# Performance work log

Measured on AMD Instinct MI355X. Metric: run time of the kernel, lower is better.

Reference implementation:

```python
import jax, jax.numpy as jnp
import numpy as np

N_LEAVES = 16384
D = 1024
L = 32


def _build_full_binary_tree(n_leaves):
    # Leaves are node ids [0, n_leaves); internal nodes are assigned ids level by
    # level bottom-up, so children always have smaller ids than their parent and
    # left_idx/right_idx are grouped contiguously per level.
    level_nodes = np.arange(n_leaves)
    nid = n_leaves
    lefts, rights = [], []
    while level_nodes.size > 1:
        lefts.append(level_nodes[0::2])
        rights.append(level_nodes[1::2])
        w = level_nodes.size // 2
        level_nodes = np.arange(nid, nid + w)
        nid += w
    return np.concatenate(lefts).astype(np.int32), np.concatenate(rights).astype(np.int32)


def setup_inputs() -> dict:
    key = jax.random.key(0)
    k_h, k_t, k_w = jax.random.split(key, 3)
    n_nodes = 2 * N_LEAVES - 1
    hidden = jax.random.normal(k_h, (n_nodes, D), dtype=jnp.float32)
    # xavier_normal-ish scales
    trans = jax.random.normal(k_t, (L, L), dtype=jnp.float32) * (2.0 / (L + L)) ** 0.5
    W_pred = jax.random.normal(k_w, (L, 2 * D), dtype=jnp.float32) * (2.0 / (2 * D + L)) ** 0.5
    b_pred = jnp.zeros((L,), dtype=jnp.float32)
    left_idx, right_idx = _build_full_binary_tree(N_LEAVES)
    return {
        "hidden": hidden,
        "trans": trans,
        "W_pred": W_pred,
        "b_pred": b_pred,
        "left_idx": jnp.asarray(left_idx),
        "right_idx": jnp.asarray(right_idx),
    }


def reference(hidden, trans, W_pred, b_pred, left_idx, right_idx):
    # hidden: [N, D] node bottom-up hidden states; N = 2*n_leaves - 1
    n_nodes, d = hidden.shape
    n_leaves = (n_nodes + 1) // 2
    num_labels = trans.shape[0]

    # collect_avg_hidden: mean over all node hidden states
    avg_h = jnp.mean(hidden, axis=0)  # [D]
    # avg_h_pred: emission = Linear(concat(h, avg_h))  -> [N, L]
    feats = jnp.concatenate(
        [hidden, jnp.broadcast_to(avg_h, hidden.shape)], axis=1
    )  # [N, 2D]
    emission = feats @ W_pred.T + b_pred  # [N, L]

    # Inside DP, bottom-up, batched by tree level. For an internal node p:
    #   inside[p, y] = logsumexp_{l,r}( emission[p,y] + trans[y,l] + inside_left[l]
    #                                   + trans[y,r] + inside_right[r] )
    # which factorizes exactly into two independent logsumexps.
    scores = jnp.zeros((n_nodes, num_labels), dtype=hidden.dtype)
    scores = scores.at[:n_leaves].set(emission[:n_leaves])

    pos = 0
    node_base = n_leaves
    width = n_leaves // 2
    while width >= 1:  # fixed log2(n_leaves) structural levels
        li = left_idx[pos:pos + width]
        ri = right_idx[pos:pos + width]
        ls = scores[li]  # [width, L]
        rs = scores[ri]  # [width, L]
        # trans[y, c] + child_score[c], logsumexp over child label c
        left_m = jax.nn.logsumexp(trans[None, :, :] + ls[:, None, :], axis=2)
        right_m = jax.nn.logsumexp(trans[None, :, :] + rs[:, None, :], axis=2)
        new = emission[node_base:node_base + width] + left_m + right_m
        scores = scores.at[node_base:node_base + width].set(new)
        pos += width
        node_base += width
        width //= 2

    return scores[n_nodes - 1]  # root inside score, [L]
```

## Files before the change

### kernel.cpp

```cpp
#include <hip/hip_runtime.h>

#define NN 32767
#define NL 16384
#define DD 1024
#define LL 32

typedef __attribute__((ext_vector_type(8))) short bf16x8;
typedef __attribute__((ext_vector_type(4))) float f32x4;

__device__ __forceinline__ short f2bf(float f) {
  union { float f; unsigned u; } x; x.f = f;
  unsigned r = x.u + 0x7FFFu + ((x.u >> 16) & 1u);
  return (short)(r >> 16);
}

__device__ __forceinline__ bf16x8 cvt8(float4 a, float4 b) {
  bf16x8 r;
  r[0] = f2bf(a.x); r[1] = f2bf(a.y); r[2] = f2bf(a.z); r[3] = f2bf(a.w);
  r[4] = f2bf(b.x); r[5] = f2bf(b.y); r[6] = f2bf(b.z); r[7] = f2bf(b.w);
  return r;
}

__device__ __forceinline__ void gld_lds16(const float* g, float* l) {
  __builtin_amdgcn_global_load_lds(
      (const __attribute__((address_space(1))) void*)g,
      (__attribute__((address_space(3))) void*)l, 16, 0, 0);
}

__global__ __launch_bounds__(256) void pack_kernel(const float* __restrict__ Wp,
                                                   short* __restrict__ Wpk) {
  int idx = blockIdx.x * 256 + threadIdx.x;
  #pragma unroll
  for (int t = 0; t < 4; ++t, idx += 16384) {
    const int j = idx & 7, m = (idx >> 3) & 3, lane = (idx >> 5) & 63, s = idx >> 11;
    const int wrow = (lane & 15) + 16 * (m & 1);
    const int wcol = (m >> 1) * 1024 + s * 32 + (lane >> 4) * 8 + j;
    Wpk[idx] = f2bf(Wp[(size_t)wrow * (2 * DD) + wcol]);
  }
}

__global__ __launch_bounds__(256) void gemm_kernel(
    const float* __restrict__ hidden, const short* __restrict__ Wpk,
    float* __restrict__ E0, float* __restrict__ gpart) {
  __shared__ float lds[4 * 3 * 1024];
  const int tid = threadIdx.x;
  const int wid = tid >> 6, lane = tid & 63;
  const int tile = blockIdx.x * 4 + wid;
  const int mrow = lane & 15, g = lane >> 4;
  const int swz = (mrow & 7) << 4;
  float* ldsw = lds + wid * 3072;

  const float* ab0; const float* ab1; const float* ab2; const float* ab3;
  {
    const int lr = lane >> 4, lc16 = (lane & 15) * 16;
    #define MKAB(I, P) { const int row = (I)*4 + lr;                         \
      const int csrc = lc16 ^ ((row & 7) << 4);                              \
      int grow = tile * 16 + row; if (grow > NN - 1) grow = NN - 1;          \
      P = hidden + (size_t)grow * DD + (csrc >> 2); }
    MKAB(0, ab0) MKAB(1, ab1) MKAB(2, ab2) MKAB(3, ab3)
    #undef MKAB
  }
  const bf16x8* wbase = (const bf16x8*)Wpk + (size_t)lane * 4;

  const int cidx00 = ((g * 32) ^ swz) >> 2;
  const int cidx01 = ((g * 32 + 16) ^ swz) >> 2;
  const int cidx10 = ((128 + g * 32) ^ swz) >> 2;
  const int cidx11 = ((128 + g * 32 + 16) ^ swz) >> 2;

  f32x4 acc0 = {0,0,0,0}, acc1 = {0,0,0,0}, acc2 = {0,0,0,0}, acc3 = {0,0,0,0};

#define STAGE_A(KC) {                                   \
    float* ld_ = ldsw + ((KC) % 3) * 1024;              \
    gld_lds16(ab0 + (KC) * 64, ld_);                    \
    gld_lds16(ab1 + (KC) * 64, ld_ + 256);              \
    gld_lds16(ab2 + (KC) * 64, ld_ + 512);              \
    gld_lds16(ab3 + (KC) * 64, ld_ + 768); }

#define LOAD_W(KC, W0,W1,W2,W3, X0,X1,X2,X3) {          \
    const bf16x8* p_ = wbase + (size_t)(2 * (KC)) * 256; \
    W0 = p_[0];   W1 = p_[1];   W2 = p_[2];   W3 = p_[3]; \
    X0 = p_[256]; X1 = p_[257]; X2 = p_[258]; X3 = p_[259]; }

#define CHUNK(KC, VM, W0,W1,W2,W3, X0,X1,X2,X3)                              \
  { if ((KC) + 2 < 16) STAGE_A((KC) + 2)                                     \
    asm volatile("s_waitcnt vmcnt(" VM ")" ::: "memory");                    \
    { const float* bc = ldsw + ((KC) % 3) * 1024 + mrow * 64;                \
      float4 fa0 = *(const float4*)(bc + cidx00);                            \
      float4 fb0 = *(const float4*)(bc + cidx01);                            \
      bf16x8 af0 = cvt8(fa0, fb0);                                           \
      acc0 = __builtin_amdgcn_mfma_f32_16x16x32_bf16(af0, W0, acc0, 0,0,0);  \
      acc1 = __builtin_amdgcn_mfma_f32_16x16x32_bf16(af0, W1, acc1, 0,0,0);  \
      acc2 = __builtin_amdgcn_mfma_f32_16x16x32_bf16(af0, W2, acc2, 0,0,0);  \
      acc3 = __builtin_amdgcn_mfma_f32_16x16x32_bf16(af0, W3, acc3, 0,0,0);  \
      float4 fa1 = *(const float4*)(bc + cidx10);                            \
      float4 fb1 = *(const float4*)(bc + cidx11);                            \
      bf16x8 af1 = cvt8(fa1, fb1);                                           \
      acc0 = __builtin_amdgcn_mfma_f32_16x16x32_bf16(af1, X0, acc0, 0,0,0);  \
      acc1 = __builtin_amdgcn_mfma_f32_16x16x32_bf16(af1, X1, acc1, 0,0,0);  \
      acc2 = __builtin_amdgcn_mfma_f32_16x16x32_bf16(af1, X2, acc2, 0,0,0);  \
      acc3 = __builtin_amdgcn_mfma_f32_16x16x32_bf16(af1, X3, acc3, 0,0,0);  \
    }                                                                        \
    if ((KC) + 2 < 16) LOAD_W((KC) + 2, W0,W1,W2,W3, X0,X1,X2,X3) }

  bf16x8 u0,u1,u2,u3,u4,u5,u6,u7, v0,v1,v2,v3,v4,v5,v6,v7;
  STAGE_A(0) STAGE_A(1)
  LOAD_W(0, u0,u1,u2,u3, u4,u5,u6,u7)
  LOAD_W(1, v0,v1,v2,v3, v4,v5,v6,v7)
  CHUNK( 0, "24", u0,u1,u2,u3, u4,u5,u6,u7)
  CHUNK( 1, "32", v0,v1,v2,v3, v4,v5,v6,v7)
  CHUNK( 2, "24", u0,u1,u2,u3, u4,u5,u6,u7)
  CHUNK( 3, "24", v0,v1,v2,v3, v4,v5,v6,v7)
  CHUNK( 4, "24", u0,u1,u2,u3, u4,u5,u6,u7)
  CHUNK( 5, "24", v0,v1,v2,v3, v4,v5,v6,v7)
  CHUNK( 6, "24", u0,u1,u2,u3, u4,u5,u6,u7)
  CHUNK( 7, "24", v0,v1,v2,v3, v4,v5,v6,v7)
  CHUNK( 8, "24", u0,u1,u2,u3, u4,u5,u6,u7)
  CHUNK( 9, "24", v0,v1,v2,v3, v4,v5,v6,v7)
  CHUNK(10, "24", u0,u1,u2,u3, u4,u5,u6,u7)
  CHUNK(11, "24", v0,v1,v2,v3, v4,v5,v6,v7)
  CHUNK(12, "24", u0,u1,u2,u3, u4,u5,u6,u7)
  CHUNK(13, "24", v0,v1,v2,v3, v4,v5,v6,v7)
  CHUNK(14, "20", u0,u1,u2,u3, u4,u5,u6,u7)
  CHUNK(15, "8",  v0,v1,v2,v3, v4,v5,v6,v7)
#undef CHUNK
#undef LOAD_W
#undef STAGE_A

  #pragma unroll
  for (int r = 0; r < 4; ++r) {
    const int srow = tile * 16 + g * 4 + r;
    if (srow < NN) {
      E0[(size_t)srow * LL + mrow]      = acc0[r];
      E0[(size_t)srow * LL + mrow + 16] = acc1[r];
    }
  }
  if (tile == 2047 && g == 3) { acc2[3] = 0.f; acc3[3] = 0.f; }
  float s2 = acc2[0] + acc2[1] + acc2[2] + acc2[3];
  float s3 = acc3[0] + acc3[1] + acc3[2] + acc3[3];
  s2 += __shfl_xor(s2, 16, 64); s2 += __shfl_xor(s2, 32, 64);
  s3 += __shfl_xor(s3, 16, 64); s3 += __shfl_xor(s3, 32, 64);
  if (lane < 32) gpart[(size_t)tile * LL + lane] = (lane < 16) ? s2 : s3;
}

__global__ __launch_bounds__(256) void cvec_kernel(
    const float* __restrict__ bp, const float* __restrict__ gpart,
    float* __restrict__ cvec) {
  const int col = blockIdx.x;
  const int tid = threadIdx.x, wid = tid >> 6, lane = tid & 63;
  float s = 0.f;
  for (int w = tid; w < 2048; w += 256) s += gpart[(size_t)w * LL + col];
  #pragma unroll
  for (int m = 1; m <= 32; m <<= 1) s += __shfl_xor(s, m, 64);
  __shared__ float red[4];
  if (lane == 0) red[wid] = s;
  __syncthreads();
  if (tid == 0)
    cvec[col] = bp[col] + (red[0] + red[1] + red[2] + red[3]) * (1.0f / (float)NN);
}

__device__ __forceinline__ float lse32(const float4* tt, const float4* sv) {
  float m = -3.0e38f;
  float4 v[8];
  #pragma unroll
  for (int i = 0; i < 8; ++i) {
    float4 t = tt[i], s = sv[i], w;
    w.x = t.x + s.x; w.y = t.y + s.y; w.z = t.z + s.z; w.w = t.w + s.w;
    v[i] = w;
    m = fmaxf(m, fmaxf(fmaxf(w.x, w.y), fmaxf(w.z, w.w)));
  }
  float ss = 0.f;
  #pragma unroll
  for (int i = 0; i < 8; ++i) {
    ss += __expf(v[i].x - m) + __expf(v[i].y - m) +
          __expf(v[i].z - m) + __expf(v[i].w - m);
  }
  return m + __logf(ss);
}

__global__ __launch_bounds__(1024) void tree_kernel(
    const float* __restrict__ E0, const float* __restrict__ cvec,
    const float* __restrict__ trans, const float* __restrict__ src,
    float* __restrict__ dst, int base1, int leafmode) {
  __shared__ float l1[16][LL], l2[8][LL], l3[4][LL];
  const int wid = threadIdx.x >> 6, lane = threadIdx.x & 63;
  const int j = lane & 31, half = lane >> 5;
  const int b = blockIdx.x, G = gridDim.x;
  float4 tt[8];
  #pragma unroll
  for (int i = 0; i < 8; ++i) tt[i] = *(const float4*)(trans + j * LL + i * 4);
  const float cj = cvec[j];
  float4 sv[8];

  {
    const int n = b * 16 + wid;
    const float* sp = src + (size_t)(2 * n + half) * LL;
    if (leafmode) {
      #pragma unroll
      for (int i = 0; i < 8; ++i) {
        float4 vv = *(const float4*)(sp + i * 4);
        float4 c4 = *(const float4*)(cvec + i * 4);
        vv.x += c4.x; vv.y += c4.y; vv.z += c4.z; vv.w += c4.w;
        sv[i] = vv;
      }
    } else {
      #pragma unroll
      for (int i = 0; i < 8; ++i) sv[i] = *(const float4*)(sp + i * 4);
    }
    float lsum = lse32(tt, sv);
    float other = __shfl_xor(lsum, 32, 64);
    float o = E0[(size_t)(base1 + n) * LL + j] + cj + lsum + other;
    if (lane < 32) l1[wid][j] = o;
  }
  __syncthreads();
  const int base2 = base1 + G * 16;
  if (wid < 8) {
    const float* sp = l1[2 * wid + half];
    #pragma unroll
    for (int i = 0; i < 8; ++i) sv[i] = *(const float4*)(sp + i * 4);
    float lsum = lse32(tt, sv);
    float other = __shfl_xor(lsum, 32, 64);
    float o = E0[(size_t)(base2 + b * 8 + wid) * LL + j] + cj + lsum + other;
    if (lane < 32) l2[wid][j] = o;
  }
  __syncthreads();
  const int base3 = base2 + G * 8;
  if (wid < 4) {
    const float* sp = l2[2 * wid + half];
    #pragma unroll
    for (int i = 0; i < 8; ++i) sv[i] = *(const float4*)(sp + i * 4);
    float lsum = lse32(tt, sv);
    float other = __shfl_xor(lsum, 32, 64);
    float o = E0[(size_t)(base3 + b * 4 + wid) * LL + j] + cj + lsum + other;
    if (lane < 32) l3[wid][j] = o;
  }
  __syncthreads();
  const int base4 = base3 + G * 4;
  if (wid < 2) {
    const float* sp = l3[2 * wid + half];
    #pragma unroll
    for (int i = 0; i < 8; ++i) sv[i] = *(const float4*)(sp + i * 4);
    float lsum = lse32(tt, sv);
    float other = __shfl_xor(lsum, 32, 64);
    float o = E0[(size_t)(base4 + b * 2 + wid) * LL + j] + cj + lsum + other;
    if (lane < 32) l1[wid][j] = o;
  }
  __syncthreads();
  const int base5 = base4 + G * 2;
  if (wid == 0) {
    const float* sp = l1[half];
    #pragma unroll
    for (int i = 0; i < 8; ++i) sv[i] = *(const float4*)(sp + i * 4);
    float lsum = lse32(tt, sv);
    float other = __shfl_xor(lsum, 32, 64);
    float o = E0[(size_t)(base5 + b) * LL + j] + cj + lsum + other;
    if (lane < 32) dst[(size_t)b * LL + j] = o;
  }
}

__global__ __launch_bounds__(512) void tail_kernel(
    const float* __restrict__ E0, const float* __restrict__ cvec,
    const float* __restrict__ trans, const float* __restrict__ S10,
    float* __restrict__ out) {
  __shared__ float t1[8][LL], t2[4][LL], t3[2][LL];
  const int wid = threadIdx.x >> 6, lane = threadIdx.x & 63;
  const int j = lane & 31, half = lane >> 5;
  float4 tt[8];
  #pragma unroll
  for (int i = 0; i < 8; ++i) tt[i] = *(const float4*)(trans + j * LL + i * 4);
  const float cj = cvec[j];
  float4 sv[8];

  {
    const float* sp = S10 + (size_t)(2 * wid + half) * LL;
    #pragma unroll
    for (int i = 0; i < 8; ++i) sv[i] = *(const float4*)(sp + i * 4);
    float lsum = lse32(tt, sv);
    float other = __shfl_xor(lsum, 32, 64);
    float o = E0[(size_t)(32752 + wid) * LL + j] + cj + lsum + other;
    if (lane < 32) t1[wid][j] = o;
  }
  __syncthreads();
  if (wid < 4) {
    const float* sp = t1[2 * wid + half];
    #pragma unroll
    for (int i = 0; i < 8; ++i) sv[i] = *(const float4*)(sp + i * 4);
    float lsum = lse32(tt, sv);
    float other = __shfl_xor(lsum, 32, 64);
    float o = E0[(size_t)(32760 + wid) * LL + j] + cj + lsum + other;
    if (lane < 32) t2[wid][j] = o;
  }
  __syncthreads();
  if (wid < 2) {
    const float* sp = t2[2 * wid + half];
    #pragma unroll
    for (int i = 0; i < 8; ++i) sv[i] = *(const float4*)(sp + i * 4);
    float lsum = lse32(tt, sv);
    float other = __shfl_xor(lsum, 32, 64);
    float o = E0[(size_t)(32764 + wid) * LL + j] + cj + lsum + other;
    if (lane < 32) t3[wid][j] = o;
  }
  __syncthreads();
  if (wid == 0) {
    const float* sp = t3[half];
    #pragma unroll
    for (int i = 0; i < 8; ++i) sv[i] = *(const float4*)(sp + i * 4);
    float lsum = lse32(tt, sv);
    float other = __shfl_xor(lsum, 32, 64);
    float o = E0[(size_t)32766 * LL + j] + cj + lsum + other;
    if (lane < 32) out[j] = o;
  }
}

extern "C" void kernel_launch(void* const* d_in, const int* in_sizes, int n_in,
                              void* d_out, int out_size, void* d_ws, size_t ws_size,
                              hipStream_t stream) {
  const float* hidden = (const float*)d_in[0];
  const float* trans  = (const float*)d_in[1];
  const float* Wp     = (const float*)d_in[2];
  const float* bp     = (const float*)d_in[3];

  float* ws    = (float*)d_ws;
  float* E0    = ws;
  float* gpart = E0 + (size_t)NN * LL;
  float* cvecb = gpart + (size_t)2048 * LL;
  float* S5    = cvecb + 32;
  float* S10   = S5 + 512 * LL;
  short* Wpk   = (short*)(S10 + 16 * LL);

  pack_kernel<<<64, 256, 0, stream>>>(Wp, Wpk);
  gemm_kernel<<<512, 256, 0, stream>>>(hidden, Wpk, E0, gpart);
  cvec_kernel<<<32, 256, 0, stream>>>(bp, gpart, cvecb);
  tree_kernel<<<512, 1024, 0, stream>>>(E0, cvecb, trans, E0, S5, 16384, 1);
  tree_kernel<<<16, 1024, 0, stream>>>(E0, cvecb, trans, S5, S10, 32256, 0);
  tail_kernel<<<1, 512, 0, stream>>>(E0, cvecb, trans, S10, (float*)d_out);
}
```

Before: 73.26 us.

## Split GEMM K across waves, drop LDS staging, fuse cvec reduction into tree kernels

The GEMM kernel now uses 1024-thread blocks in which two groups of waves each handle half of K. Each wave loads hidden directly from global memory into registers instead of staging through LDS with async copies, and the two halves are combined through shared memory. Per-block column sums are reduced to 256 partials, and the separate cvec kernel is removed: each tree and tail block recomputes cvec from those partials. This saves one launch and the LDS pipeline, but adds redundant reduction work in every tree block and loses the explicit prefetch overlap.

```diff
diff --git a/kernel.cpp b/kernel.cpp
--- a/kernel.cpp
+++ b/kernel.cpp
@@ -21,12 +21,6 @@
   return r;
 }
 
-__device__ __forceinline__ void gld_lds16(const float* g, float* l) {
-  __builtin_amdgcn_global_load_lds(
-      (const __attribute__((address_space(1))) void*)g,
-      (__attribute__((address_space(3))) void*)l, 16, 0, 0);
-}
-
 __global__ __launch_bounds__(256) void pack_kernel(const float* __restrict__ Wp,
                                                    short* __restrict__ Wpk) {
   int idx = blockIdx.x * 256 + threadIdx.x;
@@ -39,123 +33,80 @@
   }
 }
 
-__global__ __launch_bounds__(256) void gemm_kernel(
+__global__ __launch_bounds__(1024, 4) void gemm_kernel(
     const float* __restrict__ hidden, const short* __restrict__ Wpk,
-    float* __restrict__ E0, float* __restrict__ gpart) {
-  __shared__ float lds[4 * 3 * 1024];
+    float* __restrict__ E0, float* __restrict__ gpartB) {
+  __shared__ float cmb[8 * 1024];
+  __shared__ float part2[8][LL];
   const int tid = threadIdx.x;
   const int wid = tid >> 6, lane = tid & 63;
-  const int tile = blockIdx.x * 4 + wid;
+  const int wt = wid & 7, kh = wid >> 3;
+  const int tile = blockIdx.x * 8 + wt;
   const int mrow = lane & 15, g = lane >> 4;
-  const int swz = (mrow & 7) << 4;
-  float* ldsw = lds + wid * 3072;
-
-  const float* ab0; const float* ab1; const float* ab2; const float* ab3;
-  {
-    const int lr = lane >> 4, lc16 = (lane & 15) * 16;
-    #define MKAB(I, P) { const int row = (I)*4 + lr;                         \
-      const int csrc = lc16 ^ ((row & 7) << 4);                              \
-      int grow = tile * 16 + row; if (grow > NN - 1) grow = NN - 1;          \
-      P = hidden + (size_t)grow * DD + (csrc >> 2); }
-    MKAB(0, ab0) MKAB(1, ab1) MKAB(2, ab2) MKAB(3, ab3)
-    #undef MKAB
-  }
-  const bf16x8* wbase = (const bf16x8*)Wpk + (size_t)lane * 4;
-
-  const int cidx00 = ((g * 32) ^ swz) >> 2;
-  const int cidx01 = ((g * 32 + 16) ^ swz) >> 2;
-  const int cidx10 = ((128 + g * 32) ^ swz) >> 2;
-  const int cidx11 = ((128 + g * 32 + 16) ^ swz) >> 2;
+  int grow = tile * 16 + mrow;
+  if (grow > NN - 1) grow = NN - 1;
+
+  const float*  ap = hidden + (size_t)grow * DD + kh * 512 + g * 8;
+  const bf16x8* wb = (const bf16x8*)Wpk + kh * 4096 + lane * 4;
 
   f32x4 acc0 = {0,0,0,0}, acc1 = {0,0,0,0}, acc2 = {0,0,0,0}, acc3 = {0,0,0,0};
 
-#define STAGE_A(KC) {                                   \
-    float* ld_ = ldsw + ((KC) % 3) * 1024;              \
-    gld_lds16(ab0 + (KC) * 64, ld_);                    \
-    gld_lds16(ab1 + (KC) * 64, ld_ + 256);              \
-    gld_lds16(ab2 + (KC) * 64, ld_ + 512);              \
-    gld_lds16(ab3 + (KC) * 64, ld_ + 768); }
-
-#define LOAD_W(KC, W0,W1,W2,W3, X0,X1,X2,X3) {          \
-    const bf16x8* p_ = wbase + (size_t)(2 * (KC)) * 256; \
-    W0 = p_[0];   W1 = p_[1];   W2 = p_[2];   W3 = p_[3]; \
-    X0 = p_[256]; X1 = p_[257]; X2 = p_[258]; X3 = p_[259]; }
-
-#define CHUNK(KC, VM, W0,W1,W2,W3, X0,X1,X2,X3)                              \
-  { if ((KC) + 2 < 16) STAGE_A((KC) + 2)                                     \
-    asm volatile("s_waitcnt vmcnt(" VM ")" ::: "memory");                    \
-    { const float* bc = ldsw + ((KC) % 3) * 1024 + mrow * 64;                \
-      float4 fa0 = *(const float4*)(bc + cidx00);                            \
-      float4 fb0 = *(const float4*)(bc + cidx01);                            \
-      bf16x8 af0 = cvt8(fa0, fb0);                                           \
-      acc0 = __builtin_amdgcn_mfma_f32_16x16x32_bf16(af0, W0, acc0, 0,0,0);  \
-      acc1 = __builtin_amdgcn_mfma_f32_16x16x32_bf16(af0, W1, acc1, 0,0,0);  \
-      acc2 = __builtin_amdgcn_mfma_f32_16x16x32_bf16(af0, W2, acc2, 0,0,0);  \
-      acc3 = __builtin_amdgcn_mfma_f32_16x16x32_bf16(af0, W3, acc3, 0,0,0);  \
-      float4 fa1 = *(const float4*)(bc + cidx10);                            \
-      float4 fb1 = *(const float4*)(bc + cidx11);                            \
-      bf16x8 af1 = cvt8(fa1, fb1);                                           \
-      acc0 = __builtin_amdgcn_mfma_f32_16x16x32_bf16(af1, X0, acc0, 0,0,0);  \
-      acc1 = __builtin_amdgcn_mfma_f32_16x16x32_bf16(af1, X1, acc1, 0,0,0);  \
-      acc2 = __builtin_amdgcn_mfma_f32_16x16x32_bf16(af1, X2, acc2, 0,0,0);  \
-      acc3 = __builtin_amdgcn_mfma_f32_16x16x32_bf16(af1, X3, acc3, 0,0,0);  \
-    }                                                                        \
-    if ((KC) + 2 < 16) LOAD_W((KC) + 2, W0,W1,W2,W3, X0,X1,X2,X3) }
-
-  bf16x8 u0,u1,u2,u3,u4,u5,u6,u7, v0,v1,v2,v3,v4,v5,v6,v7;
-  STAGE_A(0) STAGE_A(1)
-  LOAD_W(0, u0,u1,u2,u3, u4,u5,u6,u7)
-  LOAD_W(1, v0,v1,v2,v3, v4,v5,v6,v7)
-  CHUNK( 0, "24", u0,u1,u2,u3, u4,u5,u6,u7)
-  CHUNK( 1, "32", v0,v1,v2,v3, v4,v5,v6,v7)
-  CHUNK( 2, "24", u0,u1,u2,u3, u4,u5,u6,u7)
-  CHUNK( 3, "24", v0,v1,v2,v3, v4,v5,v6,v7)
-  CHUNK( 4, "24", u0,u1,u2,u3, u4,u5,u6,u7)
-  CHUNK( 5, "24", v0,v1,v2,v3, v4,v5,v6,v7)
-  CHUNK( 6, "24", u0,u1,u2,u3, u4,u5,u6,u7)
-  CHUNK( 7, "24", v0,v1,v2,v3, v4,v5,v6,v7)
-  CHUNK( 8, "24", u0,u1,u2,u3, u4,u5,u6,u7)
-  CHUNK( 9, "24", v0,v1,v2,v3, v4,v5,v6,v7)
-  CHUNK(10, "24", u0,u1,u2,u3, u4,u5,u6,u7)
-  CHUNK(11, "24", v0,v1,v2,v3, v4,v5,v6,v7)
-  CHUNK(12, "24", u0,u1,u2,u3, u4,u5,u6,u7)
-  CHUNK(13, "24", v0,v1,v2,v3, v4,v5,v6,v7)
-  CHUNK(14, "20", u0,u1,u2,u3, u4,u5,u6,u7)
-  CHUNK(15, "8",  v0,v1,v2,v3, v4,v5,v6,v7)
-#undef CHUNK
-#undef LOAD_W
-#undef STAGE_A
-
-  #pragma unroll
-  for (int r = 0; r < 4; ++r) {
-    const int srow = tile * 16 + g * 4 + r;
-    if (srow < NN) {
-      E0[(size_t)srow * LL + mrow]      = acc0[r];
-      E0[(size_t)srow * LL + mrow + 16] = acc1[r];
+  #pragma unroll
+  for (int c = 0; c < 8; ++c) {
+    float4 a0 = *(const float4*)(ap + c * 64);
+    float4 a1 = *(const float4*)(ap + c * 64 + 4);
+    float4 a2 = *(const float4*)(ap + c * 64 + 32);
+    float4 a3 = *(const float4*)(ap + c * 64 + 36);
+    const bf16x8* p = wb + c * 512;
+    bf16x8 w0 = p[0],   w1 = p[1],   w2 = p[2],   w3 = p[3];
+    bf16x8 x0 = p[256], x1 = p[257], x2 = p[258], x3 = p[259];
+    bf16x8 af0 = cvt8(a0, a1);
+    acc0 = __builtin_amdgcn_mfma_f32_16x16x32_bf16(af0, w0, acc0, 0, 0, 0);
+    acc1 = __builtin_amdgcn_mfma_f32_16x16x32_bf16(af0, w1, acc1, 0, 0, 0);
+    acc2 = __builtin_amdgcn_mfma_f32_16x16x32_bf16(af0, w2, acc2, 0, 0, 0);
+    acc3 = __builtin_amdgcn_mfma_f32_16x16x32_bf16(af0, w3, acc3, 0, 0, 0);
+    bf16x8 af1 = cvt8(a2, a3);
+    acc0 = __builtin_amdgcn_mfma_f32_16x16x32_bf16(af1, x0, acc0, 0, 0, 0);
+    acc1 = __builtin_amdgcn_mfma_f32_16x16x32_bf16(af1, x1, acc1, 0, 0, 0);
+    acc2 = __builtin_amdgcn_mfma_f32_16x16x32_bf16(af1, x2, acc2, 0, 0, 0);
+    acc3 = __builtin_amdgcn_mfma_f32_16x16x32_bf16(af1, x3, acc3, 0, 0, 0);
+  }
+
+  float* cl = cmb + wt * 1024 + lane * 16;
+  if (kh == 1) {
+    *(f32x4*)(cl)      = acc0;
+    *(f32x4*)(cl + 4)  = acc1;
+    *(f32x4*)(cl + 8)  = acc2;
+    *(f32x4*)(cl + 12) = acc3;
+  }
+  __syncthreads();
+  if (kh == 0) {
+    acc0 += *(const f32x4*)(cl);
+    acc1 += *(const f32x4*)(cl + 4);
+    acc2 += *(const f32x4*)(cl + 8);
+    acc3 += *(const f32x4*)(cl + 12);
+    #pragma unroll
+    for (int r = 0; r < 4; ++r) {
+      const int srow = tile * 16 + g * 4 + r;
+      if (srow < NN) {
+        E0[(size_t)srow * LL + mrow]      = acc0[r];
+        E0[(size_t)srow * LL + mrow + 16] = acc1[r];
+      }
     }
-  }
-  if (tile == 2047 && g == 3) { acc2[3] = 0.f; acc3[3] = 0.f; }
-  float s2 = acc2[0] + acc2[1] + acc2[2] + acc2[3];
-  float s3 = acc3[0] + acc3[1] + acc3[2] + acc3[3];
-  s2 += __shfl_xor(s2, 16, 64); s2 += __shfl_xor(s2, 32, 64);
-  s3 += __shfl_xor(s3, 16, 64); s3 += __shfl_xor(s3, 32, 64);
-  if (lane < 32) gpart[(size_t)tile * LL + lane] = (lane < 16) ? s2 : s3;
-}
-
-__global__ __launch_bounds__(256) void cvec_kernel(
-    const float* __restrict__ bp, const float* __restrict__ gpart,
-    float* __restrict__ cvec) {
-  const int col = blockIdx.x;
-  const int tid = threadIdx.x, wid = tid >> 6, lane = tid & 63;
-  float s = 0.f;
-  for (int w = tid; w < 2048; w += 256) s += gpart[(size_t)w * LL + col];
-  #pragma unroll
-  for (int m = 1; m <= 32; m <<= 1) s += __shfl_xor(s, m, 64);
-  __shared__ float red[4];
-  if (lane == 0) red[wid] = s;
-  __syncthreads();
-  if (tid == 0)
-    cvec[col] = bp[col] + (red[0] + red[1] + red[2] + red[3]) * (1.0f / (float)NN);
+    if (tile == 2047 && g == 3) { acc2[3] = 0.f; acc3[3] = 0.f; }
+    float s2 = acc2[0] + acc2[1] + acc2[2] + acc2[3];
+    float s3 = acc3[0] + acc3[1] + acc3[2] + acc3[3];
+    s2 += __shfl_xor(s2, 16, 64); s2 += __shfl_xor(s2, 32, 64);
+    s3 += __shfl_xor(s3, 16, 64); s3 += __shfl_xor(s3, 32, 64);
+    if (lane < 32) part2[wt][lane] = (lane < 16) ? s2 : s3;
+  }
+  __syncthreads();
+  if (tid < LL) {
+    float s = 0.f;
+    #pragma unroll
+    for (int q = 0; q < 8; ++q) s += part2[q][tid];
+    gpartB[blockIdx.x * LL + tid] = s;
+  }
 }
 
 __device__ __forceinline__ float lse32(const float4* tt, const float4* sv) {
@@ -177,18 +128,42 @@
   return m + __logf(ss);
 }
 
+__device__ __forceinline__ void compute_cvec(const float* __restrict__ gpartB,
+                                             const float* __restrict__ bp,
+                                             float* cv, float (*pr)[LL]) {
+  const int tid = threadIdx.x;
+  const int j = tid & 31, r = tid >> 5;
+  float s = 0.f;
+  #pragma unroll
+  for (int q = 0; q < 8; ++q) s += gpartB[(size_t)(r + q * 32) * LL + j];
+  pr[r][j] = s;
+  __syncthreads();
+  if (tid < LL) {
+    float ss = 0.f;
+    #pragma unroll
+    for (int q = 0; q < 32; ++q) ss += pr[q][tid];
+    cv[tid] = bp[tid] + ss * (1.0f / (float)NN);
+  }
+  __syncthreads();
+}
+
 __global__ __launch_bounds__(1024) void tree_kernel(
-    const float* __restrict__ E0, const float* __restrict__ cvec,
-    const float* __restrict__ trans, const float* __restrict__ src,
-    float* __restrict__ dst, int base1, int leafmode) {
+    const float* __restrict__ E0, const float* __restrict__ gpartB,
+    const float* __restrict__ bp, const float* __restrict__ trans,
+    const float* __restrict__ src, float* __restrict__ dst,
+    int base1, int leafmode) {
+  __shared__ __align__(16) float cv[LL];
+  __shared__ float pr[32][LL];
   __shared__ float l1[16][LL], l2[8][LL], l3[4][LL];
+  compute_cvec(gpartB, bp, cv, pr);
+
   const int wid = threadIdx.x >> 6, lane = threadIdx.x & 63;
   const int j = lane & 31, half = lane >> 5;
   const int b = blockIdx.x, G = gridDim.x;
   float4 tt[8];
   #pragma unroll
   for (int i = 0; i < 8; ++i) tt[i] = *(const float4*)(trans + j * LL + i * 4);
-  const float cj = cvec[j];
+  const float cj = cv[j];
   float4 sv[8];
 
   {
@@ -198,7 +173,7 @@
       #pragma unroll
       for (int i = 0; i < 8; ++i) {
         float4 vv = *(const float4*)(sp + i * 4);
-        float4 c4 = *(const float4*)(cvec + i * 4);
+        float4 c4 = *(const float4*)(cv + i * 4);
         vv.x += c4.x; vv.y += c4.y; vv.z += c4.z; vv.w += c4.w;
         sv[i] = vv;
       }
@@ -257,20 +232,24 @@
   }
 }
 
-__global__ __launch_bounds__(512) void tail_kernel(
-    const float* __restrict__ E0, const float* __restrict__ cvec,
-    const float* __restrict__ trans, const float* __restrict__ S10,
-    float* __restrict__ out) {
+__global__ __launch_bounds__(1024) void tail_kernel(
+    const float* __restrict__ E0, const float* __restrict__ gpartB,
+    const float* __restrict__ bp, const float* __restrict__ trans,
+    const float* __restrict__ S10, float* __restrict__ out) {
+  __shared__ __align__(16) float cv[LL];
+  __shared__ float pr[32][LL];
   __shared__ float t1[8][LL], t2[4][LL], t3[2][LL];
+  compute_cvec(gpartB, bp, cv, pr);
+
   const int wid = threadIdx.x >> 6, lane = threadIdx.x & 63;
   const int j = lane & 31, half = lane >> 5;
   float4 tt[8];
   #pragma unroll
   for (int i = 0; i < 8; ++i) tt[i] = *(const float4*)(trans + j * LL + i * 4);
-  const float cj = cvec[j];
+  const float cj = cv[j];
   float4 sv[8];
 
-  {
+  if (wid < 8) {
     const float* sp = S10 + (size_t)(2 * wid + half) * LL;
     #pragma unroll
     for (int i = 0; i < 8; ++i) sv[i] = *(const float4*)(sp + i * 4);
@@ -319,18 +298,16 @@
   const float* Wp     = (const float*)d_in[2];
   const float* bp     = (const float*)d_in[3];
 
-  float* ws    = (float*)d_ws;
-  float* E0    = ws;
-  float* gpart = E0 + (size_t)NN * LL;
-  float* cvecb = gpart + (size_t)2048 * LL;
-  float* S5    = cvecb + 32;
-  float* S10   = S5 + 512 * LL;
-  short* Wpk   = (short*)(S10 + 16 * LL);
+  float* ws     = (float*)d_ws;
+  float* E0     = ws;
+  float* gpartB = E0 + (size_t)NN * LL;
+  float* S5     = gpartB + 256 * LL;
+  float* S10    = S5 + 512 * LL;
+  short* Wpk    = (short*)(S10 + 16 * LL);
 
   pack_kernel<<<64, 256, 0, stream>>>(Wp, Wpk);
-  gemm_kernel<<<512, 256, 0, stream>>>(hidden, Wpk, E0, gpart);
-  cvec_kernel<<<32, 256, 0, stream>>>(bp, gpart, cvecb);
-  tree_kernel<<<512, 1024, 0, stream>>>(E0, cvecb, trans, E0, S5, 16384, 1);
-  tree_kernel<<<16, 1024, 0, stream>>>(E0, cvecb, trans, S5, S10, 32256, 0);
-  tail_kernel<<<1, 512, 0, stream>>>(E0, cvecb, trans, S10, (float*)d_out);
-}
+  gemm_kernel<<<256, 1024, 0, stream>>>(hidden, Wpk, E0, gpartB);
+  tree_kernel<<<512, 1024, 0, stream>>>(E0, gpartB, bp, trans, E0, S5, 16384, 1);
+  tree_kernel<<<16, 1024, 0, stream>>>(E0, gpartB, bp, trans, S5, S10, 32256, 0);
+  tail_kernel<<<1, 1024, 0, stream>>>(E0, gpartB, bp, trans, S10, (float*)d_out);
+}
```

Result: slower. 81.77 us (+11.6%).

## Fuse cvec reduction and tree tail into last-block-done epilogues

Applied to the files above, without the earlier changes.

Removes the separate cvec, second tree and tail kernel launches. The GEMM's last-finishing block, detected with an atomic counter, now reduces the per-block column sums into cvec. The tree kernel's last block finishes the top nine tree levels in LDS. This cuts three launches and their inter-kernel gaps, at the cost of serialising the top levels on one block, adding atomic/fence overhead, and a large LDS allocation for every tree block.

```diff
diff --git a/kernel.cpp b/kernel.cpp
--- a/kernel.cpp
+++ b/kernel.cpp
@@ -1,4 +1,5 @@
 #include <hip/hip_runtime.h>
+
 
 #define NN 32767
 #define NL 16384
@@ -28,7 +29,9 @@
 }
 
 __global__ __launch_bounds__(256) void pack_kernel(const float* __restrict__ Wp,
-                                                   short* __restrict__ Wpk) {
+                                                   short* __restrict__ Wpk,
+                                                   unsigned* __restrict__ cnt) {
+  if (blockIdx.x == 0 && threadIdx.x == 0) { cnt[0] = 0u; cnt[1] = 0u; }
   int idx = blockIdx.x * 256 + threadIdx.x;
   #pragma unroll
   for (int t = 0; t < 4; ++t, idx += 16384) {
@@ -41,8 +44,13 @@
 
 __global__ __launch_bounds__(256) void gemm_kernel(
     const float* __restrict__ hidden, const short* __restrict__ Wpk,
-    float* __restrict__ E0, float* __restrict__ gpart) {
+    const float* __restrict__ bp, float* __restrict__ E0,
+    float* __restrict__ gpartB, float* __restrict__ cvec,
+    unsigned* __restrict__ cnt) {
   __shared__ float lds[4 * 3 * 1024];
+  __shared__ float part2[4][LL];
+  __shared__ float partC[8][LL];
+  __shared__ bool amLast;
   const int tid = threadIdx.x;
   const int wid = tid >> 6, lane = tid & 63;
   const int tile = blockIdx.x * 4 + wid;
@@ -139,23 +147,32 @@
   float s3 = acc3[0] + acc3[1] + acc3[2] + acc3[3];
   s2 += __shfl_xor(s2, 16, 64); s2 += __shfl_xor(s2, 32, 64);
   s3 += __shfl_xor(s3, 16, 64); s3 += __shfl_xor(s3, 32, 64);
-  if (lane < 32) gpart[(size_t)tile * LL + lane] = (lane < 16) ? s2 : s3;
-}
-
-__global__ __launch_bounds__(256) void cvec_kernel(
-    const float* __restrict__ bp, const float* __restrict__ gpart,
-    float* __restrict__ cvec) {
-  const int col = blockIdx.x;
-  const int tid = threadIdx.x, wid = tid >> 6, lane = tid & 63;
-  float s = 0.f;
-  for (int w = tid; w < 2048; w += 256) s += gpart[(size_t)w * LL + col];
-  #pragma unroll
-  for (int m = 1; m <= 32; m <<= 1) s += __shfl_xor(s, m, 64);
-  __shared__ float red[4];
-  if (lane == 0) red[wid] = s;
-  __syncthreads();
-  if (tid == 0)
-    cvec[col] = bp[col] + (red[0] + red[1] + red[2] + red[3]) * (1.0f / (float)NN);
+  if (lane < 32) part2[wid][lane] = (lane < 16) ? s2 : s3;
+  __syncthreads();
+  if (tid < LL) {
+    gpartB[blockIdx.x * LL + tid] =
+        part2[0][tid] + part2[1][tid] + part2[2][tid] + part2[3][tid];
+  }
+  __syncthreads();
+  if (tid == 0) {
+    __threadfence();
+    unsigned old = atomicAdd(&cnt[0], 1u);
+    amLast = (old == 511u);
+  }
+  __syncthreads();
+  if (amLast) {
+    __threadfence();
+    const int col = tid & 31, rg = tid >> 5;
+    float s = 0.f;
+    for (int r = rg; r < 512; r += 8) s += gpartB[(size_t)r * LL + col];
+    partC[rg][col] = s;
+    __syncthreads();
+    if (tid < LL) {
+      float ss = partC[0][tid] + partC[1][tid] + partC[2][tid] + partC[3][tid] +
+                 partC[4][tid] + partC[5][tid] + partC[6][tid] + partC[7][tid];
+      cvec[tid] = bp[tid] + ss * (1.0f / (float)NN);
+    }
+  }
 }
 
 __device__ __forceinline__ float lse32(const float4* tt, const float4* sv) {
@@ -179,9 +196,11 @@
 
 __global__ __launch_bounds__(1024) void tree_kernel(
     const float* __restrict__ E0, const float* __restrict__ cvec,
-    const float* __restrict__ trans, const float* __restrict__ src,
-    float* __restrict__ dst, int base1, int leafmode) {
+    const float* __restrict__ trans, float* __restrict__ S5,
+    float* __restrict__ out, unsigned* __restrict__ cnt) {
   __shared__ float l1[16][LL], l2[8][LL], l3[4][LL];
+  __shared__ float ts[511 * LL];
+  __shared__ bool amLast;
   const int wid = threadIdx.x >> 6, lane = threadIdx.x & 63;
   const int j = lane & 31, half = lane >> 5;
   const int b = blockIdx.x, G = gridDim.x;
@@ -190,21 +209,17 @@
   for (int i = 0; i < 8; ++i) tt[i] = *(const float4*)(trans + j * LL + i * 4);
   const float cj = cvec[j];
   float4 sv[8];
+  const int base1 = NL;
 
   {
     const int n = b * 16 + wid;
-    const float* sp = src + (size_t)(2 * n + half) * LL;
-    if (leafmode) {
-      #pragma unroll
-      for (int i = 0; i < 8; ++i) {
-        float4 vv = *(const float4*)(sp + i * 4);
-        float4 c4 = *(const float4*)(cvec + i * 4);
-        vv.x += c4.x; vv.y += c4.y; vv.z += c4.z; vv.w += c4.w;
-        sv[i] = vv;
-      }
-    } else {
-      #pragma unroll
-      for (int i = 0; i < 8; ++i) sv[i] = *(const float4*)(sp + i * 4);
+    const float* sp = E0 + (size_t)(2 * n + half) * LL;
+    #pragma unroll
+    for (int i = 0; i < 8; ++i) {
+      float4 vv = *(const float4*)(sp + i * 4);
+      float4 c4 = *(const float4*)(cvec + i * 4);
+      vv.x += c4.x; vv.y += c4.y; vv.z += c4.z; vv.w += c4.w;
+      sv[i] = vv;
     }
     float lsum = lse32(tt, sv);
     float other = __shfl_xor(lsum, 32, 64);
@@ -253,61 +268,39 @@
     float lsum = lse32(tt, sv);
     float other = __shfl_xor(lsum, 32, 64);
     float o = E0[(size_t)(base5 + b) * LL + j] + cj + lsum + other;
-    if (lane < 32) dst[(size_t)b * LL + j] = o;
-  }
-}
-
-__global__ __launch_bounds__(512) void tail_kernel(
-    const float* __restrict__ E0, const float* __restrict__ cvec,
-    const float* __restrict__ trans, const float* __restrict__ S10,
-    float* __restrict__ out) {
-  __shared__ float t1[8][LL], t2[4][LL], t3[2][LL];
-  const int wid = threadIdx.x >> 6, lane = threadIdx.x & 63;
-  const int j = lane & 31, half = lane >> 5;
-  float4 tt[8];
-  #pragma unroll
-  for (int i = 0; i < 8; ++i) tt[i] = *(const float4*)(trans + j * LL + i * 4);
-  const float cj = cvec[j];
-  float4 sv[8];
-
-  {
-    const float* sp = S10 + (size_t)(2 * wid + half) * LL;
-    #pragma unroll
-    for (int i = 0; i < 8; ++i) sv[i] = *(const float4*)(sp + i * 4);
-    float lsum = lse32(tt, sv);
-    float other = __shfl_xor(lsum, 32, 64);
-    float o = E0[(size_t)(32752 + wid) * LL + j] + cj + lsum + other;
-    if (lane < 32) t1[wid][j] = o;
-  }
-  __syncthreads();
-  if (wid < 4) {
-    const float* sp = t1[2 * wid + half];
-    #pragma unroll
-    for (int i = 0; i < 8; ++i) sv[i] = *(const float4*)(sp + i * 4);
-    float lsum = lse32(tt, sv);
-    float other = __shfl_xor(lsum, 32, 64);
-    float o = E0[(size_t)(32760 + wid) * LL + j] + cj + lsum + other;
-    if (lane < 32) t2[wid][j] = o;
-  }
-  __syncthreads();
-  if (wid < 2) {
-    const float* sp = t2[2 * wid + half];
-    #pragma unroll
-    for (int i = 0; i < 8; ++i) sv[i] = *(const float4*)(sp + i * 4);
-    float lsum = lse32(tt, sv);
-    float other = __shfl_xor(lsum, 32, 64);
-    float o = E0[(size_t)(32764 + wid) * LL + j] + cj + lsum + other;
-    if (lane < 32) t3[wid][j] = o;
-  }
-  __syncthreads();
-  if (wid == 0) {
-    const float* sp = t3[half];
-    #pragma unroll
-    for (int i = 0; i < 8; ++i) sv[i] = *(const float4*)(sp + i * 4);
-    float lsum = lse32(tt, sv);
-    float other = __shfl_xor(lsum, 32, 64);
-    float o = E0[(size_t)32766 * LL + j] + cj + lsum + other;
-    if (lane < 32) out[j] = o;
+    if (lane < 32) S5[(size_t)b * LL + j] = o;
+  }
+  __syncthreads();
+  if (threadIdx.x == 0) {
+    __threadfence();
+    unsigned old = atomicAdd(&cnt[1], 1u);
+    amLast = (old == 511u);
+  }
+  __syncthreads();
+  if (!amLast) return;
+  __threadfence();
+
+  int width = 256, pnode = 32256, cIdxBase = -1;
+  while (width >= 1) {
+    for (int n = wid; n < width; n += 16) {
+      const float* sp = (cIdxBase < 0)
+          ? (S5 + (size_t)(2 * n + half) * LL)
+          : (ts + (size_t)(cIdxBase + 2 * n + half) * LL);
+      #pragma unroll
+      for (int i = 0; i < 8; ++i) sv[i] = *(const float4*)(sp + i * 4);
+      float lsum = lse32(tt, sv);
+      float other = __shfl_xor(lsum, 32, 64);
+      if (lane < 32) {
+        const int node = pnode + n;
+        float o = E0[(size_t)node * LL + j] + cj + lsum + other;
+        ts[(size_t)(node - 32256) * LL + j] = o;
+        if (node == NN - 1) out[j] = o;
+      }
+    }
+    __syncthreads();
+    cIdxBase = pnode - 32256;
+    pnode += width;
+    width >>= 1;
   }
 }
 
@@ -319,18 +312,15 @@
   const float* Wp     = (const float*)d_in[2];
   const float* bp     = (const float*)d_in[3];
 
-  float* ws    = (float*)d_ws;
-  float* E0    = ws;
-  float* gpart = E0 + (size_t)NN * LL;
-  float* cvecb = gpart + (size_t)2048 * LL;
-  float* S5    = cvecb + 32;
-  float* S10   = S5 + 512 * LL;
-  short* Wpk   = (short*)(S10 + 16 * LL);
-
-  pack_kernel<<<64, 256, 0, stream>>>(Wp, Wpk);
-  gemm_kernel<<<512, 256, 0, stream>>>(hidden, Wpk, E0, gpart);
-  cvec_kernel<<<32, 256, 0, stream>>>(bp, gpart, cvecb);
-  tree_kernel<<<512, 1024, 0, stream>>>(E0, cvecb, trans, E0, S5, 16384, 1);
-  tree_kernel<<<16, 1024, 0, stream>>>(E0, cvecb, trans, S5, S10, 32256, 0);
-  tail_kernel<<<1, 512, 0, stream>>>(E0, cvecb, trans, S10, (float*)d_out);
-}
+  float* ws     = (float*)d_ws;
+  float* E0     = ws;
+  float* gpartB = E0 + (size_t)NN * LL;
+  float* cvecb  = gpartB + 512 * LL;
+  float* S5     = cvecb + 32;
+  short* Wpk    = (short*)(S5 + 512 * LL);
+  unsigned* cnt = (unsigned*)(Wpk + 65536);
+
+  pack_kernel<<<64, 256, 0, stream>>>(Wp, Wpk, cnt);
+  gemm_kernel<<<512, 256, 0, stream>>>(hidden, Wpk, bp, E0, gpartB, cvecb, cnt);
+  tree_kernel<<<512, 1024, 0, stream>>>(E0, cvecb, trans, S5, (float*)d_out, cnt);
+}
```

New measurement: 153.7 us. 110% more time.

## Fuse cvec reduction into tree kernels and collapse tree levels into two launches

Applied to the files above, without the earlier changes.

Removes the separate cvec reduction kernel. Each tree block now recomputes the column-mean vector from gpart in shared memory. The tree DP is regrouped into one 256-block kernel covering six levels and one single-block tail kernel covering the remaining eight levels, down from three tree launches. This cuts launch count and inter-kernel gaps, at the cost of redundant cvec work in every block and fewer blocks in the first tree stage.

```diff
diff --git a/kernel.cpp b/kernel.cpp
--- a/kernel.cpp
+++ b/kernel.cpp
@@ -1,4 +1,5 @@
 #include <hip/hip_runtime.h>
+
 
 #define NN 32767
 #define NL 16384
@@ -142,22 +143,6 @@
   if (lane < 32) gpart[(size_t)tile * LL + lane] = (lane < 16) ? s2 : s3;
 }
 
-__global__ __launch_bounds__(256) void cvec_kernel(
-    const float* __restrict__ bp, const float* __restrict__ gpart,
-    float* __restrict__ cvec) {
-  const int col = blockIdx.x;
-  const int tid = threadIdx.x, wid = tid >> 6, lane = tid & 63;
-  float s = 0.f;
-  for (int w = tid; w < 2048; w += 256) s += gpart[(size_t)w * LL + col];
-  #pragma unroll
-  for (int m = 1; m <= 32; m <<= 1) s += __shfl_xor(s, m, 64);
-  __shared__ float red[4];
-  if (lane == 0) red[wid] = s;
-  __syncthreads();
-  if (tid == 0)
-    cvec[col] = bp[col] + (red[0] + red[1] + red[2] + red[3]) * (1.0f / (float)NN);
-}
-
 __device__ __forceinline__ float lse32(const float4* tt, const float4* sv) {
   float m = -3.0e38f;
   float4 v[8];
@@ -177,137 +162,149 @@
   return m + __logf(ss);
 }
 
-__global__ __launch_bounds__(1024) void tree_kernel(
-    const float* __restrict__ E0, const float* __restrict__ cvec,
-    const float* __restrict__ trans, const float* __restrict__ src,
-    float* __restrict__ dst, int base1, int leafmode) {
-  __shared__ float l1[16][LL], l2[8][LL], l3[4][LL];
+__device__ __forceinline__ void compute_cvec(const float* __restrict__ gpart,
+                                             const float* __restrict__ bp,
+                                             float* cv, float (*pr)[LL]) {
+  const int tid = threadIdx.x;
+  const int j = tid & 31, r = tid >> 5;
+  float s = 0.f;
+  #pragma unroll 8
+  for (int q = 0; q < 64; ++q) s += gpart[(size_t)(r + q * 32) * LL + j];
+  pr[r][j] = s;
+  __syncthreads();
+  if (tid < LL) {
+    float ss = 0.f;
+    #pragma unroll
+    for (int q = 0; q < 32; ++q) ss += pr[q][tid];
+    cv[tid] = bp[tid] + ss * (1.0f / (float)NN);
+  }
+  __syncthreads();
+}
+
+__global__ __launch_bounds__(1024) void treeA_kernel(
+    const float* __restrict__ E0, const float* __restrict__ gpart,
+    const float* __restrict__ bp, const float* __restrict__ trans,
+    float* __restrict__ S) {
+  __shared__ __align__(16) float cv[LL];
+  __shared__ float pr[32][LL];
+  __shared__ float l1[32][LL], l2[16][LL], l3[8][LL], l4[4][LL], l5[2][LL];
+  compute_cvec(gpart, bp, cv, pr);
+
   const int wid = threadIdx.x >> 6, lane = threadIdx.x & 63;
   const int j = lane & 31, half = lane >> 5;
-  const int b = blockIdx.x, G = gridDim.x;
+  const int b = blockIdx.x;
   float4 tt[8];
   #pragma unroll
   for (int i = 0; i < 8; ++i) tt[i] = *(const float4*)(trans + j * LL + i * 4);
-  const float cj = cvec[j];
+  const float cj = cv[j];
   float4 sv[8];
 
-  {
-    const int n = b * 16 + wid;
-    const float* sp = src + (size_t)(2 * n + half) * LL;
-    if (leafmode) {
-      #pragma unroll
-      for (int i = 0; i < 8; ++i) {
-        float4 vv = *(const float4*)(sp + i * 4);
-        float4 c4 = *(const float4*)(cvec + i * 4);
-        vv.x += c4.x; vv.y += c4.y; vv.z += c4.z; vv.w += c4.w;
-        sv[i] = vv;
-      }
-    } else {
-      #pragma unroll
-      for (int i = 0; i < 8; ++i) sv[i] = *(const float4*)(sp + i * 4);
+  #pragma unroll
+  for (int k = wid; k < 32; k += 16) {
+    const int n = b * 32 + k;
+    const float* sp = E0 + (size_t)(2 * n + half) * LL;
+    #pragma unroll
+    for (int i = 0; i < 8; ++i) {
+      float4 vv = *(const float4*)(sp + i * 4);
+      float4 c4 = *(const float4*)(cv + i * 4);
+      vv.x += c4.x; vv.y += c4.y; vv.z += c4.z; vv.w += c4.w;
+      sv[i] = vv;
     }
     float lsum = lse32(tt, sv);
     float other = __shfl_xor(lsum, 32, 64);
-    float o = E0[(size_t)(base1 + n) * LL + j] + cj + lsum + other;
-    if (lane < 32) l1[wid][j] = o;
-  }
-  __syncthreads();
-  const int base2 = base1 + G * 16;
+    float o = E0[(size_t)(16384 + n) * LL + j] + cj + lsum + other;
+    if (lane < 32) l1[k][j] = o;
+  }
+  __syncthreads();
+  if (wid < 16) {
+    const float* sp = l1[2 * wid + half];
+    #pragma unroll
+    for (int i = 0; i < 8; ++i) sv[i] = *(const float4*)(sp + i * 4);
+    float lsum = lse32(tt, sv);
+    float other = __shfl_xor(lsum, 32, 64);
+    float o = E0[(size_t)(24576 + b * 16 + wid) * LL + j] + cj + lsum + other;
+    if (lane < 32) l2[wid][j] = o;
+  }
+  __syncthreads();
   if (wid < 8) {
-    const float* sp = l1[2 * wid + half];
-    #pragma unroll
-    for (int i = 0; i < 8; ++i) sv[i] = *(const float4*)(sp + i * 4);
-    float lsum = lse32(tt, sv);
-    float other = __shfl_xor(lsum, 32, 64);
-    float o = E0[(size_t)(base2 + b * 8 + wid) * LL + j] + cj + lsum + other;
-    if (lane < 32) l2[wid][j] = o;
-  }
-  __syncthreads();
-  const int base3 = base2 + G * 8;
+    const float* sp = l2[2 * wid + half];
+    #pragma unroll
+    for (int i = 0; i < 8; ++i) sv[i] = *(const float4*)(sp + i * 4);
+    float lsum = lse32(tt, sv);
+    float other = __shfl_xor(lsum, 32, 64);
+    float o = E0[(size_t)(28672 + b * 8 + wid) * LL + j] + cj + lsum + other;
+    if (lane < 32) l3[wid][j] = o;
+  }
+  __syncthreads();
   if (wid < 4) {
-    const float* sp = l2[2 * wid + half];
-    #pragma unroll
-    for (int i = 0; i < 8; ++i) sv[i] = *(const float4*)(sp + i * 4);
-    float lsum = lse32(tt, sv);
-    float other = __shfl_xor(lsum, 32, 64);
-    float o = E0[(size_t)(base3 + b * 4 + wid) * LL + j] + cj + lsum + other;
-    if (lane < 32) l3[wid][j] = o;
-  }
-  __syncthreads();
-  const int base4 = base3 + G * 4;
+    const float* sp = l3[2 * wid + half];
+    #pragma unroll
+    for (int i = 0; i < 8; ++i) sv[i] = *(const float4*)(sp + i * 4);
+    float lsum = lse32(tt, sv);
+    float other = __shfl_xor(lsum, 32, 64);
+    float o = E0[(size_t)(30720 + b * 4 + wid) * LL + j] + cj + lsum + other;
+    if (lane < 32) l4[wid][j] = o;
+  }
+  __syncthreads();
   if (wid < 2) {
-    const float* sp = l3[2 * wid + half];
-    #pragma unroll
-    for (int i = 0; i < 8; ++i) sv[i] = *(const float4*)(sp + i * 4);
-    float lsum = lse32(tt, sv);
-    float other = __shfl_xor(lsum, 32, 64);
-    float o = E0[(size_t)(base4 + b * 2 + wid) * LL + j] + cj + lsum + other;
-    if (lane < 32) l1[wid][j] = o;
-  }
-  __syncthreads();
-  const int base5 = base4 + G * 2;
+    const float* sp = l4[2 * wid + half];
+    #pragma unroll
+    for (int i = 0; i < 8; ++i) sv[i] = *(const float4*)(sp + i * 4);
+    float lsum = lse32(tt, sv);
+    float other = __shfl_xor(lsum, 32, 64);
+    float o = E0[(size_t)(31744 + b * 2 + wid) * LL + j] + cj + lsum + other;
+    if (lane < 32) l5[wid][j] = o;
+  }
+  __syncthreads();
   if (wid == 0) {
-    const float* sp = l1[half];
-    #pragma unroll
-    for (int i = 0; i < 8; ++i) sv[i] = *(const float4*)(sp + i * 4);
-    float lsum = lse32(tt, sv);
-    float other = __shfl_xor(lsum, 32, 64);
-    float o = E0[(size_t)(base5 + b) * LL + j] + cj + lsum + other;
-    if (lane < 32) dst[(size_t)b * LL + j] = o;
-  }
-}
-
-__global__ __launch_bounds__(512) void tail_kernel(
-    const float* __restrict__ E0, const float* __restrict__ cvec,
-    const float* __restrict__ trans, const float* __restrict__ S10,
-    float* __restrict__ out) {
-  __shared__ float t1[8][LL], t2[4][LL], t3[2][LL];
+    const float* sp = l5[half];
+    #pragma unroll
+    for (int i = 0; i < 8; ++i) sv[i] = *(const float4*)(sp + i * 4);
+    float lsum = lse32(tt, sv);
+    float other = __shfl_xor(lsum, 32, 64);
+    float o = E0[(size_t)(32256 + b) * LL + j] + cj + lsum + other;
+    if (lane < 32) S[(size_t)b * LL + j] = o;
+  }
+}
+
+__global__ __launch_bounds__(1024) void tail_kernel(
+    const float* __restrict__ E0, const float* __restrict__ gpart,
+    const float* __restrict__ bp, const float* __restrict__ trans,
+    const float* __restrict__ S, float* __restrict__ out) {
+  __shared__ __align__(16) float cv[LL];
+  __shared__ float pr[32][LL];
+  __shared__ float ts[255 * LL];
+  compute_cvec(gpart, bp, cv, pr);
+
   const int wid = threadIdx.x >> 6, lane = threadIdx.x & 63;
   const int j = lane & 31, half = lane >> 5;
   float4 tt[8];
   #pragma unroll
   for (int i = 0; i < 8; ++i) tt[i] = *(const float4*)(trans + j * LL + i * 4);
-  const float cj = cvec[j];
+  const float cj = cv[j];
   float4 sv[8];
 
-  {
-    const float* sp = S10 + (size_t)(2 * wid + half) * LL;
-    #pragma unroll
-    for (int i = 0; i < 8; ++i) sv[i] = *(const float4*)(sp + i * 4);
-    float lsum = lse32(tt, sv);
-    float other = __shfl_xor(lsum, 32, 64);
-    float o = E0[(size_t)(32752 + wid) * LL + j] + cj + lsum + other;
-    if (lane < 32) t1[wid][j] = o;
-  }
-  __syncthreads();
-  if (wid < 4) {
-    const float* sp = t1[2 * wid + half];
-    #pragma unroll
-    for (int i = 0; i < 8; ++i) sv[i] = *(const float4*)(sp + i * 4);
-    float lsum = lse32(tt, sv);
-    float other = __shfl_xor(lsum, 32, 64);
-    float o = E0[(size_t)(32760 + wid) * LL + j] + cj + lsum + other;
-    if (lane < 32) t2[wid][j] = o;
-  }
-  __syncthreads();
-  if (wid < 2) {
-    const float* sp = t2[2 * wid + half];
-    #pragma unroll
-    for (int i = 0; i < 8; ++i) sv[i] = *(const float4*)(sp + i * 4);
-    float lsum = lse32(tt, sv);
-    float other = __shfl_xor(lsum, 32, 64);
-    float o = E0[(size_t)(32764 + wid) * LL + j] + cj + lsum + other;
-    if (lane < 32) t3[wid][j] = o;
-  }
-  __syncthreads();
-  if (wid == 0) {
-    const float* sp = t3[half];
-    #pragma unroll
-    for (int i = 0; i < 8; ++i) sv[i] = *(const float4*)(sp + i * 4);
-    float lsum = lse32(tt, sv);
-    float other = __shfl_xor(lsum, 32, 64);
-    float o = E0[(size_t)32766 * LL + j] + cj + lsum + other;
-    if (lane < 32) out[j] = o;
+  int width = 128, pnode = 32512, cIdxBase = -1;
+  while (width >= 1) {
+    for (int n = wid; n < width; n += 16) {
+      const float* sp = (cIdxBase < 0)
+          ? (S + (size_t)(2 * n + half) * LL)
+          : (ts + (size_t)(cIdxBase + 2 * n + half) * LL);
+      #pragma unroll
+      for (int i = 0; i < 8; ++i) sv[i] = *(const float4*)(sp + i * 4);
+      float lsum = lse32(tt, sv);
+      float other = __shfl_xor(lsum, 32, 64);
+      if (lane < 32) {
+        const int node = pnode + n;
+        float o = E0[(size_t)node * LL + j] + cj + lsum + other;
+        ts[(size_t)(node - 32512) * LL + j] = o;
+        if (node == NN - 1) out[j] = o;
+      }
+    }
+    __syncthreads();
+    cIdxBase = pnode - 32512;
+    pnode += width;
+    width >>= 1;
   }
 }
 
@@ -322,15 +319,11 @@
   float* ws    = (float*)d_ws;
   float* E0    = ws;
   float* gpart = E0 + (size_t)NN * LL;
-  float* cvecb = gpart + (size_t)2048 * LL;
-  float* S5    = cvecb + 32;
-  float* S10   = S5 + 512 * LL;
-  short* Wpk   = (short*)(S10 + 16 * LL);
+  float* S     = gpart + (size_t)2048 * LL;
+  short* Wpk   = (short*)(S + 256 * LL);
 
   pack_kernel<<<64, 256, 0, stream>>>(Wp, Wpk);
   gemm_kernel<<<512, 256, 0, stream>>>(hidden, Wpk, E0, gpart);
-  cvec_kernel<<<32, 256, 0, stream>>>(bp, gpart, cvecb);
-  tree_kernel<<<512, 1024, 0, stream>>>(E0, cvecb, trans, E0, S5, 16384, 1);
-  tree_kernel<<<16, 1024, 0, stream>>>(E0, cvecb, trans, S5, S10, 32256, 0);
-  tail_kernel<<<1, 512, 0, stream>>>(E0, cvecb, trans, S10, (float*)d_out);
-}
+  treeA_kernel<<<256, 1024, 0, stream>>>(E0, gpart, bp, trans, S);
+  tail_kernel<<<1, 1024, 0, stream>>>(E0, gpart, bp, trans, S, (float*)d_out);
+}
```

After: 89.88 us. +22.7%, slower.
